# Optimization experiments

Hardware: AMD Instinct MI355X
Metric: run time of the kernel (lower is better)

## Reference

```python
import jax, jax.numpy as jnp
import numpy as np

QMAX = 127.0  # int8 symmetric
EPS = 1e-8

def _quant_dequant(v, axis):
    # symmetric int8 fake-quant along `axis` (per-row for weights, per-token for acts)
    scale = jnp.max(jnp.abs(v), axis=axis, keepdims=True) / QMAX
    scale = jnp.maximum(scale, EPS)
    q = jnp.clip(jnp.round(v / scale), -QMAX, QMAX)
    return q * scale

def _ste(v, axis):
    # straight-through estimator: identity gradient through quantization
    return v + jax.lax.stop_gradient(_quant_dequant(v, axis) - v)

def setup_inputs() -> dict:
    key = jax.random.key(0)
    k1, k2, k3 = jax.random.split(key, 3)
    H, I = 2048, 5632
    x = jax.random.normal(k1, (4, 2048, H), dtype=jnp.float32)
    # nn.Linear weight layout: [out_features, in_features]
    w_gate_up = jax.random.normal(k2, (2 * I, H), dtype=jnp.float32) * (H ** -0.5)
    w_down = jax.random.normal(k3, (H, I), dtype=jnp.float32) * (I ** -0.5)
    return {"x": x, "w_gate_up": w_gate_up, "w_down": w_down}

def reference(x, w_gate_up, w_down):
    I = w_down.shape[1]
    # QLinear #1: quantize act per-token, weight per-out-channel, dequant matmul
    xq = _ste(x, axis=-1)                       # [B,S,H]
    w1q = _ste(w_gate_up, axis=-1)              # [2I,H]
    gate_up = jnp.einsum('bsh,oh->bso', xq, w1q)  # [B,S,2I]
    gate, up = gate_up[..., :I], gate_up[..., I:]
    h = jax.nn.silu(gate) * up                  # SwiGLU, [B,S,I]
    # QLinear #2
    hq = _ste(h, axis=-1)
    w2q = _ste(w_down, axis=-1)                 # [H,I]
    return jnp.einsum('bsi,oi->bso', hq, w2q)   # [B,S,H]
```

## Files before the change

kernel.cpp:

```cpp
#include <hip/hip_runtime.h>
#include <hip/hip_bf16.h>
#include <stdint.h>

#define H_DIM 2048
#define I_DIM 5632
#define M_DIM 8192
#define N1_DIM (2 * I_DIM)

typedef __attribute__((ext_vector_type(4))) int i32x4;

__device__ __forceinline__ void gload16(const void* g, void* l) {
  __builtin_amdgcn_global_load_lds(
      reinterpret_cast<const __attribute__((address_space(1))) uint32_t*>(
          reinterpret_cast<uintptr_t>(g)),
      reinterpret_cast<__attribute__((address_space(3))) uint32_t*>(
          reinterpret_cast<uintptr_t>(l)),
      16, 0, 0);
}

#define BAR()                                \
  do {                                       \
    asm volatile("" ::: "memory");           \
    __builtin_amdgcn_s_barrier();            \
    asm volatile("" ::: "memory");           \
  } while (0)

__global__ __launch_bounds__(256) void quant_rows_f32(
    const float* __restrict__ in, int8_t* __restrict__ q,
    float* __restrict__ scl, int rowlen) {
  const int row = blockIdx.x;
  const int tid = threadIdx.x;
  const float* rp = in + (size_t)row * rowlen;
  float m = 0.f;
  for (int i = tid * 4; i < rowlen; i += 1024) {
    const float4 v = *reinterpret_cast<const float4*>(rp + i);
    m = fmaxf(m, fmaxf(fmaxf(fabsf(v.x), fabsf(v.y)),
                       fmaxf(fabsf(v.z), fabsf(v.w))));
  }
#pragma unroll
  for (int o = 32; o; o >>= 1) m = fmaxf(m, __shfl_xor(m, o));
  __shared__ float wm[4];
  if ((tid & 63) == 0) wm[tid >> 6] = m;
  __syncthreads();
  m = fmaxf(fmaxf(wm[0], wm[1]), fmaxf(wm[2], wm[3]));
  const float scale = fmaxf(m / 127.0f, 1e-8f);
  const float inv = 1.0f / scale;
  if (tid == 0) scl[row] = scale;
  int8_t* qp = q + (size_t)row * rowlen;
  for (int i = tid * 4; i < rowlen; i += 1024) {
    const float4 v = *reinterpret_cast<const float4*>(rp + i);
    const int a = (int)rintf(fminf(fmaxf(v.x * inv, -127.f), 127.f));
    const int b = (int)rintf(fminf(fmaxf(v.y * inv, -127.f), 127.f));
    const int c = (int)rintf(fminf(fmaxf(v.z * inv, -127.f), 127.f));
    const int d = (int)rintf(fminf(fmaxf(v.w * inv, -127.f), 127.f));
    *reinterpret_cast<int*>(qp + i) =
        (a & 255) | ((b & 255) << 8) | ((c & 255) << 16) | (d << 24);
  }
}

__global__ __launch_bounds__(256) void quant_h_rows(
    const __hip_bfloat16* __restrict__ h, const int* __restrict__ amax,
    int8_t* __restrict__ q, float* __restrict__ scl) {
  const int row = blockIdx.x;
  const int tid = threadIdx.x;
  const float scale = fmaxf(__int_as_float(amax[row]) / 127.0f, 1e-8f);
  const float inv = 1.0f / scale;
  if (tid == 0) scl[row] = scale;
  const __hip_bfloat16* rp = h + (size_t)row * I_DIM;
  int8_t* qp = q + (size_t)row * I_DIM;
  for (int i = tid * 8; i < I_DIM; i += 2048) {
    const uint4 v = *reinterpret_cast<const uint4*>(rp + i);
    const uint32_t w[4] = {v.x, v.y, v.z, v.w};
    int pk0 = 0, pk1 = 0;
#pragma unroll
    for (int j = 0; j < 8; ++j) {
      const float f =
          __uint_as_float(((w[j >> 1] >> ((j & 1) * 16)) & 0xffffu) << 16);
      const int qv = (int)rintf(fminf(fmaxf(f * inv, -127.f), 127.f));
      if (j < 4) pk0 |= (qv & 255) << ((j & 3) * 8);
      else       pk1 |= (qv & 255) << ((j & 3) * 8);
    }
    *reinterpret_cast<int2*>(qp + i) = make_int2(pk0, pk1);
  }
}

__global__ __launch_bounds__(512, 2) void gemm1_silu(
    const int8_t* __restrict__ qx, const float* __restrict__ sx,
    const int8_t* __restrict__ qw, const float* __restrict__ sw,
    __hip_bfloat16* __restrict__ h, int* __restrict__ hmax) {
  __shared__ int8_t lds[131072];
  const int tid = threadIdx.x;
  const int lane = tid & 63;
  const int wid = tid >> 6;
  const int wr = wid >> 2;
  const int wc = wid & 3;
  const int c16 = lane & 15;
  const int kq = lane >> 4;
  const int r7 = lane & 7;
  const int lr = lane >> 3;
  const int sslot = ((lane & 7) ^ lr) << 4;
  const int sl0 = (kq ^ r7) << 4;
  const int sl1 = ((4 + kq) ^ r7) << 4;

  const int nwg = gridDim.x;
  const int id = blockIdx.x;
  const int swz = (id & 7) * (nwg >> 3) + (id >> 3);
  const int NBN = I_DIM / 128;
  const int bm = swz / NBN;
  const int bn = swz % NBN;

  const size_t goffA = (size_t)(bm * 256 + wid * 8 + lr) * H_DIM + sslot;
  const size_t goffG = (size_t)(bn * 128 + wid * 8 + lr) * H_DIM + sslot;
  const size_t goffU = goffG + (size_t)I_DIM * H_DIM;
  const int ldsAw = wid * 8 * 128;
  const int ldsBw = 65536 + wid * 8 * 128;

  i32x4 acc[2][4][2][2] = {};

#define STAGE_A1(half, t)                                                      \
  do {                                                                         \
    const int _b = ((t) & 1) * 32768;                                          \
    _Pragma("unroll") for (int ld = 0; ld < 2; ++ld)                           \
        gload16(qx + goffA + (size_t)((half)*128 + ld * 64) * H_DIM +          \
                    (size_t)(t) * 128,                                         \
                lds + _b + ldsAw + ((half)*128 + ld * 64) * 128);              \
  } while (0)

#define STAGE_B1(half, t)                                                      \
  do {                                                                         \
    const int _b = ((t) & 1) * 32768;                                          \
    const int8_t* _s = (half) ? (qw + goffU) : (qw + goffG);                   \
    _Pragma("unroll") for (int ld = 0; ld < 2; ++ld)                           \
        gload16(_s + (size_t)(ld * 64) * H_DIM + (size_t)(t) * 128,            \
                lds + _b + ldsBw + ((half)*128 + ld * 64) * 128);              \
  } while (0)

#define LOAD_A1(MH)                                                            \
  do {                                                                         \
    _Pragma("unroll") for (int m = 0; m < 4; ++m) {                            \
      const int ar = (MH)*128 + wr * 64 + m * 16 + c16;                        \
      a[m][0] = *reinterpret_cast<const i32x4*>(lds + cb + ar * 128 + sl0);    \
      a[m][1] = *reinterpret_cast<const i32x4*>(lds + cb + ar * 128 + sl1);    \
    }                                                                          \
  } while (0)

#define LOAD_B1(NH)                                                            \
  do {                                                                         \
    _Pragma("unroll") for (int n = 0; n < 2; ++n) {                            \
      const int br = (NH)*128 + wc * 32 + n * 16 + c16;                        \
      b[NH][n][0] =                                                            \
          *reinterpret_cast<const i32x4*>(lds + 65536 + cb + br * 128 + sl0);  \
      b[NH][n][1] =                                                            \
          *reinterpret_cast<const i32x4*>(lds + 65536 + cb + br * 128 + sl1);  \
    }                                                                          \
  } while (0)

#define MFMA_Q1(MH, NH)                                                        \
  do {                                                                         \
    __builtin_amdgcn_s_setprio(1);                                             \
    _Pragma("unroll") for (int kk = 0; kk < 2; ++kk)                           \
        _Pragma("unroll") for (int m = 0; m < 4; ++m)                          \
            _Pragma("unroll") for (int n = 0; n < 2; ++n) acc[MH][m][NH][n] =  \
        __builtin_amdgcn_mfma_i32_16x16x64_i8(a[m][kk], b[NH][n][kk],          \
                                              acc[MH][m][NH][n], 0, 0, 0);     \
    __builtin_amdgcn_s_setprio(0);                                             \
  } while (0)

  const int KT = H_DIM / 128;
  STAGE_A1(0, 0); STAGE_B1(0, 0); STAGE_A1(1, 0); STAGE_B1(1, 0);
  STAGE_A1(0, 1); STAGE_B1(0, 1);
  asm volatile("s_waitcnt vmcnt(4)" ::: "memory");
  BAR();

#pragma unroll 1
  for (int t = 0; t < KT; ++t) {
    const int cb = (t & 1) * 32768;
    i32x4 a[4][2], b[2][2][2];
    LOAD_A1(0); LOAD_B1(0);
    if (t + 1 < KT) STAGE_A1(1, t + 1);
    BAR();
    MFMA_Q1(0, 0);
    BAR();
    LOAD_B1(1);
    if (t + 1 < KT) STAGE_B1(1, t + 1);
    BAR();
    MFMA_Q1(0, 1);
    BAR();
    LOAD_A1(1);
    if (t + 2 < KT) STAGE_A1(0, t + 2);
    BAR();
    MFMA_Q1(1, 0);
    BAR();
    if (t + 2 < KT) STAGE_B1(0, t + 2);
    BAR();
    MFMA_Q1(1, 1);
    if (t + 2 < KT) asm volatile("s_waitcnt vmcnt(4)" ::: "memory");
    else            asm volatile("s_waitcnt vmcnt(0)" ::: "memory");
    BAR();
  }

  const int row0 = bm * 256 + wr * 64 + kq * 4;
  const int col0 = bn * 128 + wc * 32 + c16;
#pragma unroll
  for (int mh = 0; mh < 2; ++mh) {
#pragma unroll
    for (int m = 0; m < 4; ++m) {
#pragma unroll
      for (int r = 0; r < 4; ++r) {
        const int row = row0 + mh * 128 + m * 16 + r;
        const float sxr = sx[row];
        float rmax = 0.f;
#pragma unroll
        for (int n = 0; n < 2; ++n) {
          const int col = col0 + n * 16;
          const float g = (float)acc[mh][m][0][n][r] * (sxr * sw[col]);
          const float u = (float)acc[mh][m][1][n][r] * (sxr * sw[I_DIM + col]);
          const float hv = g / (1.f + __expf(-g)) * u;
          h[(size_t)row * I_DIM + col] = __float2bfloat16(hv);
          rmax = fmaxf(rmax, fabsf(hv));
        }
#pragma unroll
        for (int o = 1; o < 16; o <<= 1)
          rmax = fmaxf(rmax, __shfl_xor(rmax, o));
        if (c16 == 0) atomicMax(hmax + row, __float_as_int(rmax));
      }
    }
  }
}

__global__ __launch_bounds__(512, 2) void gemm2(
    const int8_t* __restrict__ qh, const float* __restrict__ sh,
    const int8_t* __restrict__ qw, const float* __restrict__ sw,
    float* __restrict__ out) {
  __shared__ int8_t lds[131072];
  const int tid = threadIdx.x;
  const int lane = tid & 63;
  const int wid = tid >> 6;
  const int wr = wid >> 2;
  const int wc = wid & 3;
  const int c16 = lane & 15;
  const int kq = lane >> 4;
  const int r7 = lane & 7;
  const int lr = lane >> 3;
  const int sslot = ((lane & 7) ^ lr) << 4;
  const int sl0 = (kq ^ r7) << 4;
  const int sl1 = ((4 + kq) ^ r7) << 4;

  const int nwg = gridDim.x;
  const int id = blockIdx.x;
  const int swz = (id & 7) * (nwg >> 3) + (id >> 3);
  const int NBN = H_DIM / 256;
  const int bm = swz / NBN;
  const int bn = swz % NBN;

  const size_t goffA = (size_t)(bm * 256 + wid * 8 + lr) * I_DIM + sslot;
  const size_t goffB = (size_t)(bn * 256 + wid * 8 + lr) * I_DIM + sslot;
  const int ldsAw = wid * 8 * 128;
  const int ldsBw = 65536 + wid * 8 * 128;

  i32x4 acc[2][4][2][2] = {};

#define STAGE_A2(half, t)                                                      \
  do {                                                                         \
    const int _b = ((t) & 1) * 32768;                                          \
    _Pragma("unroll") for (int ld = 0; ld < 2; ++ld)                           \
        gload16(qh + goffA + (size_t)((half)*128 + ld * 64) * I_DIM +          \
                    (size_t)(t) * 128,                                         \
                lds + _b + ldsAw + ((half)*128 + ld * 64) * 128);              \
  } while (0)

#define STAGE_B2(half, t)                                                      \
  do {                                                                         \
    const int _b = ((t) & 1) * 32768;                                          \
    _Pragma("unroll") for (int ld = 0; ld < 2; ++ld)                           \
        gload16(qw + goffB + (size_t)((half)*128 + ld * 64) * I_DIM +          \
                    (size_t)(t) * 128,                                         \
                lds + _b + ldsBw + ((half)*128 + ld * 64) * 128);              \
  } while (0)

#define LOAD_A2(MH)                                                            \
  do {                                                                         \
    _Pragma("unroll") for (int m = 0; m < 4; ++m) {                            \
      const int ar = (MH)*128 + wr * 64 + m * 16 + c16;                        \
      a[m][0] = *reinterpret_cast<const i32x4*>(lds + cb + ar * 128 + sl0);    \
      a[m][1] = *reinterpret_cast<const i32x4*>(lds + cb + ar * 128 + sl1);    \
    }                                                                          \
  } while (0)

#define LOAD_B2(NH)                                                            \
  do {                                                                         \
    _Pragma("unroll") for (int n = 0; n < 2; ++n) {                            \
      const int br = (NH)*128 + wc * 32 + n * 16 + c16;                        \
      b[NH][n][0] =                                                            \
          *reinterpret_cast<const i32x4*>(lds + 65536 + cb + br * 128 + sl0);  \
      b[NH][n][1] =                                                            \
          *reinterpret_cast<const i32x4*>(lds + 65536 + cb + br * 128 + sl1);  \
    }                                                                          \
  } while (0)

#define MFMA_Q2(MH, NH)                                                        \
  do {                                                                         \
    __builtin_amdgcn_s_setprio(1);                                             \
    _Pragma("unroll") for (int kk = 0; kk < 2; ++kk)                           \
        _Pragma("unroll") for (int m = 0; m < 4; ++m)                          \
            _Pragma("unroll") for (int n = 0; n < 2; ++n) acc[MH][m][NH][n] =  \
        __builtin_amdgcn_mfma_i32_16x16x64_i8(a[m][kk], b[NH][n][kk],          \
                                              acc[MH][m][NH][n], 0, 0, 0);     \
    __builtin_amdgcn_s_setprio(0);                                             \
  } while (0)

  const int KT = I_DIM / 128;
  STAGE_A2(0, 0); STAGE_B2(0, 0); STAGE_A2(1, 0); STAGE_B2(1, 0);
  STAGE_A2(0, 1); STAGE_B2(0, 1);
  asm volatile("s_waitcnt vmcnt(4)" ::: "memory");
  BAR();

#pragma unroll 1
  for (int t = 0; t < KT; ++t) {
    const int cb = (t & 1) * 32768;
    i32x4 a[4][2], b[2][2][2];
    LOAD_A2(0); LOAD_B2(0);
    if (t + 1 < KT) STAGE_A2(1, t + 1);
    BAR();
    MFMA_Q2(0, 0);
    BAR();
    LOAD_B2(1);
    if (t + 1 < KT) STAGE_B2(1, t + 1);
    BAR();
    MFMA_Q2(0, 1);
    BAR();
    LOAD_A2(1);
    if (t + 2 < KT) STAGE_A2(0, t + 2);
    BAR();
    MFMA_Q2(1, 0);
    BAR();
    if (t + 2 < KT) STAGE_B2(0, t + 2);
    BAR();
    MFMA_Q2(1, 1);
    if (t + 2 < KT) asm volatile("s_waitcnt vmcnt(4)" ::: "memory");
    else            asm volatile("s_waitcnt vmcnt(0)" ::: "memory");
    BAR();
  }

  const int row0 = bm * 256 + wr * 64 + kq * 4;
  const int col0 = bn * 256 + wc * 32 + c16;
#pragma unroll
  for (int mh = 0; mh < 2; ++mh) {
#pragma unroll
    for (int m = 0; m < 4; ++m) {
#pragma unroll
      for (int r = 0; r < 4; ++r) {
        const int row = row0 + mh * 128 + m * 16 + r;
        const float shr = sh[row];
#pragma unroll
        for (int nh = 0; nh < 2; ++nh) {
#pragma unroll
          for (int n = 0; n < 2; ++n) {
            const int col = col0 + nh * 128 + n * 16;
            out[(size_t)row * H_DIM + col] =
                (float)acc[mh][m][nh][n][r] * (shr * sw[col]);
          }
        }
      }
    }
  }
}

extern "C" void kernel_launch(void* const* d_in, const int* in_sizes, int n_in,
                              void* d_out, int out_size, void* d_ws, size_t ws_size,
                              hipStream_t stream) {
  (void)in_sizes; (void)n_in; (void)out_size; (void)ws_size;
  const float* x  = (const float*)d_in[0];
  const float* w1 = (const float*)d_in[1];
  const float* w2 = (const float*)d_in[2];
  float* out = (float*)d_out;

  size_t off = 0;
  auto alloc = [&](size_t n) {
    void* p = (char*)d_ws + off;
    off += (n + 255) & ~(size_t)255;
    return p;
  };
  int8_t* qx  = (int8_t*)alloc((size_t)M_DIM * H_DIM);
  int8_t* qw1 = (int8_t*)alloc((size_t)N1_DIM * H_DIM);
  int8_t* qw2 = (int8_t*)alloc((size_t)H_DIM * I_DIM);
  int8_t* qh  = (int8_t*)alloc((size_t)M_DIM * I_DIM);
  __hip_bfloat16* hb = (__hip_bfloat16*)alloc((size_t)M_DIM * I_DIM * 2);
  float* sx  = (float*)alloc((size_t)M_DIM * 4);
  float* sw1 = (float*)alloc((size_t)N1_DIM * 4);
  float* sw2 = (float*)alloc((size_t)H_DIM * 4);
  float* shs = (float*)alloc((size_t)M_DIM * 4);
  int* hmax  = (int*)alloc((size_t)M_DIM * 4);

  hipMemsetAsync(hmax, 0, (size_t)M_DIM * 4, stream);
  quant_rows_f32<<<M_DIM, 256, 0, stream>>>(x, qx, sx, H_DIM);
  quant_rows_f32<<<N1_DIM, 256, 0, stream>>>(w1, qw1, sw1, H_DIM);
  quant_rows_f32<<<H_DIM, 256, 0, stream>>>(w2, qw2, sw2, I_DIM);
  gemm1_silu<<<(M_DIM / 256) * (I_DIM / 128), 512, 0, stream>>>(
      qx, sx, qw1, sw1, hb, hmax);
  quant_h_rows<<<M_DIM, 256, 0, stream>>>(hb, hmax, qh, shs);
  gemm2<<<(M_DIM / 256) * (H_DIM / 256), 512, 0, stream>>>(
      qh, shs, qw2, sw2, out);
}
```

Before: 459.4 us.

## Use inline-asm LDS reads with manual lgkmcnt waits to overlap reads with MFMA

Replaces compiler-generated LDS fragment loads with inline ds_read_b128 using precomputed base addresses. The B halves and the second A half are read earlier, and explicit lgkmcnt waits plus sched_barriers let MFMAs start on the first fragments while later reads are still in flight. The goal is to hide LDS latency behind matrix math in both GEMM kernels. In exchange it holds more fragments in registers, which risks register pressure with 2 waves/SIMD. Because the asm reads are volatile with no real memory dependency, correctness relies entirely on the hand-placed waitcnts and barriers.

```diff
diff --git a/kernel.cpp b/kernel.cpp
--- a/kernel.cpp
+++ b/kernel.cpp
@@ -18,12 +18,22 @@
       16, 0, 0);
 }
 
-#define BAR()                                \
-  do {                                       \
-    asm volatile("" ::: "memory");           \
-    __builtin_amdgcn_s_barrier();            \
-    asm volatile("" ::: "memory");           \
-  } while (0)
+__device__ __forceinline__ i32x4 ds_read128(uint32_t addr) {
+  i32x4 d;
+  asm volatile("s_mov_b32 m0, -1\n\tds_read_b128 %0, %1"
+               : "=v"(d)
+               : "v"(addr));
+  return d;
+}
+
+#define MEMF() asm volatile("" ::: "memory")
+#define BAR()                      \
+  do {                             \
+    MEMF();                        \
+    __builtin_amdgcn_s_barrier();  \
+    MEMF();                        \
+  } while (0)
+#define SCHEDB() __builtin_amdgcn_sched_barrier(0)
 
 __global__ __launch_bounds__(256) void quant_rows_f32(
     const float* __restrict__ in, int8_t* __restrict__ q,
@@ -92,12 +102,8 @@
   const int tid = threadIdx.x;
   const int lane = tid & 63;
   const int wid = tid >> 6;
-  const int wr = wid >> 2;
-  const int wc = wid & 3;
-  const int c16 = lane & 15;
-  const int kq = lane >> 4;
-  const int r7 = lane & 7;
-  const int lr = lane >> 3;
+  const int wr = wid >> 2, wc = wid & 3;
+  const int c16 = lane & 15, kq = lane >> 4, r7 = lane & 7, lr = lane >> 3;
   const int sslot = ((lane & 7) ^ lr) << 4;
   const int sl0 = (kq ^ r7) << 4;
   const int sl1 = ((4 + kq) ^ r7) << 4;
@@ -106,8 +112,7 @@
   const int id = blockIdx.x;
   const int swz = (id & 7) * (nwg >> 3) + (id >> 3);
   const int NBN = I_DIM / 128;
-  const int bm = swz / NBN;
-  const int bn = swz % NBN;
+  const int bm = swz / NBN, bn = swz % NBN;
 
   const size_t goffA = (size_t)(bm * 256 + wid * 8 + lr) * H_DIM + sslot;
   const size_t goffG = (size_t)(bn * 128 + wid * 8 + lr) * H_DIM + sslot;
@@ -115,6 +120,12 @@
   const int ldsAw = wid * 8 * 128;
   const int ldsBw = 65536 + wid * 8 * 128;
 
+  const uint32_t L = (uint32_t)(uintptr_t)(void*)&lds[0];
+  const uint32_t aB0 = L + (wr * 64 + c16) * 128 + sl0;
+  const uint32_t aB1 = L + (wr * 64 + c16) * 128 + sl1;
+  const uint32_t bB0 = L + 65536 + (wc * 32 + c16) * 128 + sl0;
+  const uint32_t bB1 = L + 65536 + (wc * 32 + c16) * 128 + sl1;
+
   i32x4 acc[2][4][2][2] = {};
 
 #define STAGE_A1(half, t)                                                      \
@@ -135,33 +146,29 @@
                 lds + _b + ldsBw + ((half)*128 + ld * 64) * 128);              \
   } while (0)
 
-#define LOAD_A1(MH)                                                            \
+#define RD_A(MH)                                                               \
   do {                                                                         \
     _Pragma("unroll") for (int m = 0; m < 4; ++m) {                            \
-      const int ar = (MH)*128 + wr * 64 + m * 16 + c16;                        \
-      a[m][0] = *reinterpret_cast<const i32x4*>(lds + cb + ar * 128 + sl0);    \
-      a[m][1] = *reinterpret_cast<const i32x4*>(lds + cb + ar * 128 + sl1);    \
+      a[MH][m][0] = ds_read128(ab0 + (MH)*16384 + m * 2048);                   \
+      a[MH][m][1] = ds_read128(ab1 + (MH)*16384 + m * 2048);                   \
     }                                                                          \
   } while (0)
 
-#define LOAD_B1(NH)                                                            \
+#define RD_B(NH)                                                               \
   do {                                                                         \
     _Pragma("unroll") for (int n = 0; n < 2; ++n) {                            \
-      const int br = (NH)*128 + wc * 32 + n * 16 + c16;                        \
-      b[NH][n][0] =                                                            \
-          *reinterpret_cast<const i32x4*>(lds + 65536 + cb + br * 128 + sl0);  \
-      b[NH][n][1] =                                                            \
-          *reinterpret_cast<const i32x4*>(lds + 65536 + cb + br * 128 + sl1);  \
+      b[NH][n][0] = ds_read128(bb0 + (NH)*16384 + n * 2048);                   \
+      b[NH][n][1] = ds_read128(bb1 + (NH)*16384 + n * 2048);                   \
     }                                                                          \
   } while (0)
 
-#define MFMA_Q1(MH, NH)                                                        \
+#define MFMA_Q(MH, NH)                                                         \
   do {                                                                         \
     __builtin_amdgcn_s_setprio(1);                                             \
     _Pragma("unroll") for (int kk = 0; kk < 2; ++kk)                           \
         _Pragma("unroll") for (int m = 0; m < 4; ++m)                          \
             _Pragma("unroll") for (int n = 0; n < 2; ++n) acc[MH][m][NH][n] =  \
-        __builtin_amdgcn_mfma_i32_16x16x64_i8(a[m][kk], b[NH][n][kk],          \
+        __builtin_amdgcn_mfma_i32_16x16x64_i8(a[MH][m][kk], b[NH][n][kk],      \
                                               acc[MH][m][NH][n], 0, 0, 0);     \
     __builtin_amdgcn_s_setprio(0);                                             \
   } while (0)
@@ -175,25 +182,34 @@
 #pragma unroll 1
   for (int t = 0; t < KT; ++t) {
     const int cb = (t & 1) * 32768;
-    i32x4 a[4][2], b[2][2][2];
-    LOAD_A1(0); LOAD_B1(0);
+    const uint32_t ab0 = aB0 + cb, ab1 = aB1 + cb;
+    const uint32_t bb0 = bB0 + cb, bb1 = bB1 + cb;
+    i32x4 a[2][4][2], b[2][2][2];
+    RD_A(0); RD_B(0); RD_B(1);
+    MEMF();
     if (t + 1 < KT) STAGE_A1(1, t + 1);
     BAR();
-    MFMA_Q1(0, 0);
-    BAR();
-    LOAD_B1(1);
+    asm volatile("s_waitcnt lgkmcnt(4)" ::: "memory");
+    SCHEDB();
+    MFMA_Q(0, 0);
+    BAR();
+    RD_A(1);
+    MEMF();
     if (t + 1 < KT) STAGE_B1(1, t + 1);
     BAR();
-    MFMA_Q1(0, 1);
-    BAR();
-    LOAD_A1(1);
+    asm volatile("s_waitcnt lgkmcnt(8)" ::: "memory");
+    SCHEDB();
+    MFMA_Q(0, 1);
+    BAR();
     if (t + 2 < KT) STAGE_A1(0, t + 2);
     BAR();
-    MFMA_Q1(1, 0);
+    asm volatile("s_waitcnt lgkmcnt(0)" ::: "memory");
+    SCHEDB();
+    MFMA_Q(1, 0);
     BAR();
     if (t + 2 < KT) STAGE_B1(0, t + 2);
     BAR();
-    MFMA_Q1(1, 1);
+    MFMA_Q(1, 1);
     if (t + 2 < KT) asm volatile("s_waitcnt vmcnt(4)" ::: "memory");
     else            asm volatile("s_waitcnt vmcnt(0)" ::: "memory");
     BAR();
@@ -236,12 +252,8 @@
   const int tid = threadIdx.x;
   const int lane = tid & 63;
   const int wid = tid >> 6;
-  const int wr = wid >> 2;
-  const int wc = wid & 3;
-  const int c16 = lane & 15;
-  const int kq = lane >> 4;
-  const int r7 = lane & 7;
-  const int lr = lane >> 3;
+  const int wr = wid >> 2, wc = wid & 3;
+  const int c16 = lane & 15, kq = lane >> 4, r7 = lane & 7, lr = lane >> 3;
   const int sslot = ((lane & 7) ^ lr) << 4;
   const int sl0 = (kq ^ r7) << 4;
   const int sl1 = ((4 + kq) ^ r7) << 4;
@@ -250,13 +262,18 @@
   const int id = blockIdx.x;
   const int swz = (id & 7) * (nwg >> 3) + (id >> 3);
   const int NBN = H_DIM / 256;
-  const int bm = swz / NBN;
-  const int bn = swz % NBN;
+  const int bm = swz / NBN, bn = swz % NBN;
 
   const size_t goffA = (size_t)(bm * 256 + wid * 8 + lr) * I_DIM + sslot;
   const size_t goffB = (size_t)(bn * 256 + wid * 8 + lr) * I_DIM + sslot;
   const int ldsAw = wid * 8 * 128;
   const int ldsBw = 65536 + wid * 8 * 128;
+
+  const uint32_t L = (uint32_t)(uintptr_t)(void*)&lds[0];
+  const uint32_t aB0 = L + (wr * 64 + c16) * 128 + sl0;
+  const uint32_t aB1 = L + (wr * 64 + c16) * 128 + sl1;
+  const uint32_t bB0 = L + 65536 + (wc * 32 + c16) * 128 + sl0;
+  const uint32_t bB1 = L + 65536 + (wc * 32 + c16) * 128 + sl1;
 
   i32x4 acc[2][4][2][2] = {};
 
@@ -278,37 +295,6 @@
                 lds + _b + ldsBw + ((half)*128 + ld * 64) * 128);              \
   } while (0)
 
-#define LOAD_A2(MH)                                                            \
-  do {                                                                         \
-    _Pragma("unroll") for (int m = 0; m < 4; ++m) {                            \
-      const int ar = (MH)*128 + wr * 64 + m * 16 + c16;                        \
-      a[m][0] = *reinterpret_cast<const i32x4*>(lds + cb + ar * 128 + sl0);    \
-      a[m][1] = *reinterpret_cast<const i32x4*>(lds + cb + ar * 128 + sl1);    \
-    }                                                                          \
-  } while (0)
-
-#define LOAD_B2(NH)                                                            \
-  do {                                                                         \
-    _Pragma("unroll") for (int n = 0; n < 2; ++n) {                            \
-      const int br = (NH)*128 + wc * 32 + n * 16 + c16;                        \
-      b[NH][n][0] =                                                            \
-          *reinterpret_cast<const i32x4*>(lds + 65536 + cb + br * 128 + sl0);  \
-      b[NH][n][1] =                                                            \
-          *reinterpret_cast<const i32x4*>(lds + 65536 + cb + br * 128 + sl1);  \
-    }                                                                          \
-  } while (0)
-
-#define MFMA_Q2(MH, NH)                                                        \
-  do {                                                                         \
-    __builtin_amdgcn_s_setprio(1);                                             \
-    _Pragma("unroll") for (int kk = 0; kk < 2; ++kk)                           \
-        _Pragma("unroll") for (int m = 0; m < 4; ++m)                          \
-            _Pragma("unroll") for (int n = 0; n < 2; ++n) acc[MH][m][NH][n] =  \
-        __builtin_amdgcn_mfma_i32_16x16x64_i8(a[m][kk], b[NH][n][kk],          \
-                                              acc[MH][m][NH][n], 0, 0, 0);     \
-    __builtin_amdgcn_s_setprio(0);                                             \
-  } while (0)
-
   const int KT = I_DIM / 128;
   STAGE_A2(0, 0); STAGE_B2(0, 0); STAGE_A2(1, 0); STAGE_B2(1, 0);
   STAGE_A2(0, 1); STAGE_B2(0, 1);
@@ -318,25 +304,34 @@
 #pragma unroll 1
   for (int t = 0; t < KT; ++t) {
     const int cb = (t & 1) * 32768;
-    i32x4 a[4][2], b[2][2][2];
-    LOAD_A2(0); LOAD_B2(0);
+    const uint32_t ab0 = aB0 + cb, ab1 = aB1 + cb;
+    const uint32_t bb0 = bB0 + cb, bb1 = bB1 + cb;
+    i32x4 a[2][4][2], b[2][2][2];
+    RD_A(0); RD_B(0); RD_B(1);
+    MEMF();
     if (t + 1 < KT) STAGE_A2(1, t + 1);
     BAR();
-    MFMA_Q2(0, 0);
-    BAR();
-    LOAD_B2(1);
+    asm volatile("s_waitcnt lgkmcnt(4)" ::: "memory");
+    SCHEDB();
+    MFMA_Q(0, 0);
+    BAR();
+    RD_A(1);
+    MEMF();
     if (t + 1 < KT) STAGE_B2(1, t + 1);
     BAR();
-    MFMA_Q2(0, 1);
-    BAR();
-    LOAD_A2(1);
+    asm volatile("s_waitcnt lgkmcnt(8)" ::: "memory");
+    SCHEDB();
+    MFMA_Q(0, 1);
+    BAR();
     if (t + 2 < KT) STAGE_A2(0, t + 2);
     BAR();
-    MFMA_Q2(1, 0);
+    asm volatile("s_waitcnt lgkmcnt(0)" ::: "memory");
+    SCHEDB();
+    MFMA_Q(1, 0);
     BAR();
     if (t + 2 < KT) STAGE_B2(0, t + 2);
     BAR();
-    MFMA_Q2(1, 1);
+    MFMA_Q(1, 1);
     if (t + 2 < KT) asm volatile("s_waitcnt vmcnt(4)" ::: "memory");
     else            asm volatile("s_waitcnt vmcnt(0)" ::: "memory");
     BAR();
```

New measurement: 465.5 us. No clear change (+1.3%).
